# Kernel tuning notes

Hardware: AMD Instinct MI355X
Metric: run time of the kernel (lower is better)

The kernel has to match this reference:

```python
import jax, jax.numpy as jnp
import numpy as np

HEAD, DIM_IN, HDIM = 8, 256, 64
B, N = 4, 2048


def setup_inputs() -> dict:
    key = jax.random.key(0)
    k1, k2, k3, k4 = jax.random.split(key, 4)
    # xavier_uniform gain=1.414 bounds
    def xavier(k, shape, fan_in, fan_out):
        bound = 1.414 * np.sqrt(6.0 / (fan_in + fan_out))
        return jax.random.uniform(k, shape, jnp.float32, -bound, bound)
    h = jax.random.normal(k1, (B, N, DIM_IN), jnp.float32)
    w = xavier(k2, (HEAD, DIM_IN, HDIM), DIM_IN, HDIM)
    a_src = xavier(k3, (HEAD, HDIM, 1), HDIM, 1)
    a_dst = xavier(k4, (HEAD, HDIM, 1), HDIM, 1)
    b = jnp.zeros((HDIM,), jnp.float32)
    return {"h": h, "w": w, "a_src": a_src, "a_dst": a_dst, "b": b}


def reference(h, w, a_src, a_dst, b):
    # h: [B,N,Din], w: [H,Din,O] -> h_: [B,H,N,O]
    h_ = jnp.einsum("bnd,hdo->bhno", h, w)
    # additive attention logits per node: [B,H,N]
    src = jnp.einsum("bhno,ho->bhn", h_, a_src[..., 0])
    dst = jnp.einsum("bhno,ho->bhn", h_, a_dst[..., 0])
    # attn[b,h,i,j] = leaky_relu(src[i] + dst[j]); softmax over j
    logits = jax.nn.leaky_relu(src[..., :, None] + dst[..., None, :], negative_slope=0.2)
    attn = jax.nn.softmax(logits, axis=-1)  # [B,H,N,N]
    h_out = jnp.einsum("bhij,bhjo->bhio", attn, h_)
    return h_out + b
```

## Files before the change

kernel.cpp:

```cpp
#include <hip/hip_runtime.h>
#include <cstdint>
#include <cstddef>


#define HEADS 8
#define DIN   256
#define HDIM  64
#define NN    2048

typedef __attribute__((ext_vector_type(8))) _Float16 f16x8;
typedef __attribute__((ext_vector_type(2))) _Float16 f16x2;
typedef __attribute__((ext_vector_type(2))) __fp16   fp16x2;
typedef __attribute__((ext_vector_type(4))) float f32x4;

union H8 { f16x8 v; f16x2 p[4]; unsigned u[4]; };
union F2U { f16x2 h; fp16x2 q; unsigned u; };

__device__ __forceinline__ f16x2 pkrtz(float a, float b) {
  F2U t; t.q = __builtin_amdgcn_cvt_pkrtz(a, b);
  return t.h;
}
__device__ __forceinline__ unsigned pkrtz_u(float a, float b) {
  F2U t; t.q = __builtin_amdgcn_cvt_pkrtz(a, b);
  return t.u;
}

__global__ __launch_bounds__(256) void gat_prep(const float* __restrict__ w,
                                                const float* __restrict__ h,
                                                _Float16* __restrict__ wt,
                                                _Float16* __restrict__ hc) {
  const int bid = blockIdx.x;
  if (bid < 512) {
    const int idx = bid * 256 + threadIdx.x;
    const int o  = idx & 63;
    const int k  = (idx >> 6) & 255;
    const int hd = idx >> 14;
    wt[(hd * HDIM + o) * DIN + k] = (_Float16)w[idx];
  } else {
    const int idx = (bid - 512) * 256 + threadIdx.x;
    const float* p = h + (size_t)idx * 8;
    float4 x0 = ((const float4*)p)[0];
    float4 x1 = ((const float4*)p)[1];
    H8 o;
    o.p[0] = pkrtz(x0.x, x0.y); o.p[1] = pkrtz(x0.z, x0.w);
    o.p[2] = pkrtz(x1.x, x1.y); o.p[3] = pkrtz(x1.z, x1.w);
    *(f16x8*)(hc + (size_t)idx * 8) = o.v;
  }
}

__global__ __launch_bounds__(256) void gat_proj(const _Float16* __restrict__ hc,
                                                const _Float16* __restrict__ wt,
                                                const float* __restrict__ a_src,
                                                const float* __restrict__ a_dst,
                                                _Float16* __restrict__ h_t,
                                                float* __restrict__ src_s,
                                                float* __restrict__ dst_s) {
  const int head = blockIdx.x;
  const int rt   = blockIdx.y;
  const int tid  = threadIdx.x;
  const int w    = tid >> 6;
  const int lane = tid & 63;
  const int l15  = lane & 15, lg = lane >> 4;

  const int rowg = rt * 128 + w * 32;
  const _Float16* hb = hc + (size_t)rowg * DIN;
  const _Float16* wb = wt + head * (HDIM * DIN);

  f32x4 acc[2][4] = {};
#pragma unroll
  for (int kk = 0; kk < 8; ++kk) {
    const int k0 = kk * 32 + lg * 8;
    f16x8 af[2];
#pragma unroll
    for (int m = 0; m < 2; ++m)
      af[m] = *(const f16x8*)(hb + (size_t)(m * 16 + l15) * DIN + k0);
    f16x8 bfr[4];
#pragma unroll
    for (int n = 0; n < 4; ++n)
      bfr[n] = *(const f16x8*)(wb + (size_t)(n * 16 + l15) * DIN + k0);
#pragma unroll
    for (int m = 0; m < 2; ++m)
#pragma unroll
      for (int n = 0; n < 4; ++n)
        acc[m][n] = __builtin_amdgcn_mfma_f32_16x16x32_f16(af[m], bfr[n], acc[m][n], 0, 0, 0);
  }

  const int b   = (rt * 128) >> 11;
  const int nl0 = ((rt * 128) & 2047) + w * 32;
  const int bh  = b * HEADS + head;
  _Float16* hb_t = h_t + (size_t)bh * (256 * 512);
#pragma unroll
  for (int m = 0; m < 2; ++m)
#pragma unroll
    for (int n = 0; n < 4; ++n) {
      uint2 pk;
      pk.x = pkrtz_u(acc[m][n][0], acc[m][n][1]);
      pk.y = pkrtz_u(acc[m][n][2], acc[m][n][3]);
      const int j0 = nl0 + m * 16 + lg * 4;
      const int o  = n * 16 + l15;
      *(uint2*)(hb_t + (size_t)(j0 >> 3) * 512 + o * 8 + (j0 & 7)) = pk;
    }

  const float LOG2E = 1.4426950408889634f;
  float as4[4], ad4[4];
#pragma unroll
  for (int n = 0; n < 4; ++n) {
    as4[n] = a_src[head * HDIM + n * 16 + l15];
    ad4[n] = a_dst[head * HDIM + n * 16 + l15];
  }
#pragma unroll
  for (int m = 0; m < 2; ++m)
#pragma unroll
    for (int reg = 0; reg < 4; ++reg) {
      float ps = 0.f, pd = 0.f;
#pragma unroll
      for (int n = 0; n < 4; ++n) {
        float c = acc[m][n][reg];
        ps = fmaf(c, as4[n], ps);
        pd = fmaf(c, ad4[n], pd);
      }
#pragma unroll
      for (int off = 1; off <= 8; off <<= 1) {
        ps += __shfl_xor(ps, off);
        pd += __shfl_xor(pd, off);
      }
      if (l15 == 0) {
        const int nl = nl0 + m * 16 + lg * 4 + reg;
        src_s[(size_t)bh * NN + nl] = ps * LOG2E;
        dst_s[(size_t)bh * NN + nl] = pd * LOG2E;
      }
    }
}

__global__ __launch_bounds__(256) void gat_flash(const float* __restrict__ src_s,
                                                 const float* __restrict__ dst_s,
                                                 const _Float16* __restrict__ h_t,
                                                 const float* __restrict__ bias,
                                                 float* __restrict__ out) {
  const int it  = blockIdx.x;
  const int bh  = blockIdx.y;
  const int tid = threadIdx.x;
  const int w   = tid >> 6;
  const int lane = tid & 63;
  const int l15 = lane & 15, lg = lane >> 4;

  __shared__ _Float16 Ef[NN];
  __shared__ _Float16 Ff[NN];
  __shared__ float red[4];

  const float* dstp = dst_s + (size_t)bh * NN;
  const _Float16* vpan = h_t + (size_t)bh * (256 * 512);
  const _Float16* fb = vpan + lg * 512 + l15 * 8;

  float d[8];
  {
    float4 q0 = *(const float4*)(dstp + tid * 8);
    float4 q1 = *(const float4*)(dstp + tid * 8 + 4);
    d[0]=q0.x; d[1]=q0.y; d[2]=q0.z; d[3]=q0.w;
    d[4]=q1.x; d[5]=q1.y; d[6]=q1.z; d[7]=q1.w;
  }
  float dm = fmaxf(fmaxf(fmaxf(d[0],d[1]),fmaxf(d[2],d[3])),
                   fmaxf(fmaxf(d[4],d[5]),fmaxf(d[6],d[7])));
#pragma unroll
  for (int off = 32; off >= 1; off >>= 1) dm = fmaxf(dm, __shfl_xor(dm, off));
  if (lane == 0) red[w] = dm;
  __syncthreads();
  dm = fmaxf(fmaxf(red[0], red[1]), fmaxf(red[2], red[3]));

  {
    H8 e8, f8;
#pragma unroll
    for (int k = 0; k < 4; ++k) {
      float a0 = d[2*k]   - dm;
      float a1 = d[2*k+1] - dm;
      e8.p[k] = pkrtz(__builtin_amdgcn_exp2f(a0), __builtin_amdgcn_exp2f(a1));
      f8.p[k] = pkrtz(__builtin_amdgcn_exp2f(0.2f * a0),
                      __builtin_amdgcn_exp2f(0.2f * a1));
    }
    *(f16x8*)(&Ef[tid * 8]) = e8.v;
    *(f16x8*)(&Ff[tid * 8]) = f8.v;
  }
  __syncthreads();

  const float* srcp = src_s + (size_t)bh * NN + it * 128 + w * 32;
  f16x2 u2[2], v2[2];
#pragma unroll
  for (int m = 0; m < 2; ++m) {
    float sv   = srcp[m * 16 + l15];
    float smax = sv + dm;
    float mi   = fmaxf(smax, 0.2f * smax);
    float u    = __builtin_amdgcn_exp2f(smax - mi);
    float v    = __builtin_amdgcn_exp2f(fmaf(0.2f, smax, -mi));
    u2[m] = pkrtz(u, u);
    v2[m] = pkrtz(v, v);
  }

  f32x4 acc[2][4] = {};
  f32x4 accs[2]   = {};
  H8 onesU; onesU.u[0] = onesU.u[1] = onesU.u[2] = onesU.u[3] = 0x3C003C00u;
  const f16x8 ones = onesU.v;

  f16x8 V00, V01, V02, V03, V10, V11, V12, V13;
  f16x8 V20, V21, V22, V23, V30, V31, V32, V33;

#define LOADV(s, jc) do {                                              \
    const _Float16* fp_ = fb + (size_t)(jc) * 2048;                    \
    V##s##0 = *(const f16x8*)(fp_);                                    \
    V##s##1 = *(const f16x8*)(fp_ + 128);                              \
    V##s##2 = *(const f16x8*)(fp_ + 256);                              \
    V##s##3 = *(const f16x8*)(fp_ + 384);                              \
  } while (0)

#define STEP(s, jc) do {                                               \
    H8 eu_, fu_;                                                       \
    eu_.v = *(const f16x8*)(&Ef[(jc) * 32 + lg * 8]);                  \
    fu_.v = *(const f16x8*)(&Ff[(jc) * 32 + lg * 8]);                  \
    _Pragma("unroll") for (int m = 0; m < 2; ++m) {                    \
      H8 af_;                                                          \
      af_.p[0] = __builtin_elementwise_max(u2[m] * eu_.p[0], v2[m] * fu_.p[0]); \
      af_.p[1] = __builtin_elementwise_max(u2[m] * eu_.p[1], v2[m] * fu_.p[1]); \
      af_.p[2] = __builtin_elementwise_max(u2[m] * eu_.p[2], v2[m] * fu_.p[2]); \
      af_.p[3] = __builtin_elementwise_max(u2[m] * eu_.p[3], v2[m] * fu_.p[3]); \
      acc[m][0] = __builtin_amdgcn_mfma_f32_16x16x32_f16(af_.v, V##s##0, acc[m][0], 0, 0, 0); \
      acc[m][1] = __builtin_amdgcn_mfma_f32_16x16x32_f16(af_.v, V##s##1, acc[m][1], 0, 0, 0); \
      acc[m][2] = __builtin_amdgcn_mfma_f32_16x16x32_f16(af_.v, V##s##2, acc[m][2], 0, 0, 0); \
      acc[m][3] = __builtin_amdgcn_mfma_f32_16x16x32_f16(af_.v, V##s##3, acc[m][3], 0, 0, 0); \
      accs[m]   = __builtin_amdgcn_mfma_f32_16x16x32_f16(af_.v, ones, accs[m], 0, 0, 0);      \
    }                                                                  \
  } while (0)

  LOADV(0, 0);
  LOADV(1, 1);
  LOADV(2, 2);
#pragma unroll 1
  for (int t = 0; t < 60; t += 4) {
    LOADV(3, t + 3); STEP(0, t);
    LOADV(0, t + 4); STEP(1, t + 1);
    LOADV(1, t + 5); STEP(2, t + 2);
    LOADV(2, t + 6); STEP(3, t + 3);
  }
  LOADV(3, 63);
  STEP(0, 60); STEP(1, 61); STEP(2, 62); STEP(3, 63);

#undef LOADV
#undef STEP

  float bb[4];
#pragma unroll
  for (int n = 0; n < 4; ++n) bb[n] = bias[n * 16 + l15];

  float* ob = out + ((size_t)bh * NN + it * 128 + w * 32) * HDIM;
#pragma unroll
  for (int m = 0; m < 2; ++m)
#pragma unroll
    for (int reg = 0; reg < 4; ++reg) {
      const float linv = 1.0f / accs[m][reg];
      const int r = m * 16 + lg * 4 + reg;
#pragma unroll
      for (int n = 0; n < 4; ++n)
        ob[(size_t)r * HDIM + n * 16 + l15] = fmaf(acc[m][n][reg], linv, bb[n]);
    }
}

extern "C" void kernel_launch(void* const* d_in, const int* in_sizes, int n_in,
                              void* d_out, int out_size, void* d_ws, size_t ws_size,
                              hipStream_t stream) {
  const float* h     = (const float*)d_in[0];
  const float* w     = (const float*)d_in[1];
  const float* a_src = (const float*)d_in[2];
  const float* a_dst = (const float*)d_in[3];
  const float* bias  = (const float*)d_in[4];
  float* out = (float*)d_out;

  char* ws = (char*)d_ws;
  _Float16* wt  = (_Float16*)ws;
  _Float16* h_t = (_Float16*)(ws + 262144);
  float* src_s = (float*)(ws + 262144 + 8388608);
  float* dst_s = (float*)(ws + 262144 + 8388608 + 262144);

  _Float16* hcv = (_Float16*)d_out;

  hipLaunchKernelGGL(gat_prep,  dim3(1536),   dim3(256), 0, stream, w, h, wt, hcv);
  hipLaunchKernelGGL(gat_proj,  dim3(8, 64),  dim3(256), 0, stream,
                     hcv, wt, a_src, a_dst, h_t, src_s, dst_s);
  hipLaunchKernelGGL(gat_flash, dim3(16, 32), dim3(256), 0, stream,
                     src_s, dst_s, h_t, bias, out);
}
```

Before: 49.58 us.

## Deepen V-fragment prefetch to eight stages and prioritize MFMA issue

Raises the register-level software pipeline for V fragments from four to eight slots, so global loads are issued seven chunks ahead instead of three. The STEP body now computes both attention-fragment operands before issuing all ten MFMAs in one burst, and wraps that burst in s_setprio to raise wave priority. The aim is to hide more global load latency and keep the matrix unit busy. The cost is 64 extra VGPRs for V buffers, which could lower occupancy or cause spills.

```diff
diff --git a/kernel.cpp b/kernel.cpp
--- a/kernel.cpp
+++ b/kernel.cpp
@@ -202,6 +202,8 @@
 
   f16x8 V00, V01, V02, V03, V10, V11, V12, V13;
   f16x8 V20, V21, V22, V23, V30, V31, V32, V33;
+  f16x8 V40, V41, V42, V43, V50, V51, V52, V53;
+  f16x8 V60, V61, V62, V63, V70, V71, V72, V73;
 
 #define LOADV(s, jc) do {                                              \
     const _Float16* fp_ = fb + (size_t)(jc) * 2048;                    \
@@ -215,32 +217,45 @@
     H8 eu_, fu_;                                                       \
     eu_.v = *(const f16x8*)(&Ef[(jc) * 32 + lg * 8]);                  \
     fu_.v = *(const f16x8*)(&Ff[(jc) * 32 + lg * 8]);                  \
-    _Pragma("unroll") for (int m = 0; m < 2; ++m) {                    \
-      H8 af_;                                                          \
-      af_.p[0] = __builtin_elementwise_max(u2[m] * eu_.p[0], v2[m] * fu_.p[0]); \
-      af_.p[1] = __builtin_elementwise_max(u2[m] * eu_.p[1], v2[m] * fu_.p[1]); \
-      af_.p[2] = __builtin_elementwise_max(u2[m] * eu_.p[2], v2[m] * fu_.p[2]); \
-      af_.p[3] = __builtin_elementwise_max(u2[m] * eu_.p[3], v2[m] * fu_.p[3]); \
-      acc[m][0] = __builtin_amdgcn_mfma_f32_16x16x32_f16(af_.v, V##s##0, acc[m][0], 0, 0, 0); \
-      acc[m][1] = __builtin_amdgcn_mfma_f32_16x16x32_f16(af_.v, V##s##1, acc[m][1], 0, 0, 0); \
-      acc[m][2] = __builtin_amdgcn_mfma_f32_16x16x32_f16(af_.v, V##s##2, acc[m][2], 0, 0, 0); \
-      acc[m][3] = __builtin_amdgcn_mfma_f32_16x16x32_f16(af_.v, V##s##3, acc[m][3], 0, 0, 0); \
-      accs[m]   = __builtin_amdgcn_mfma_f32_16x16x32_f16(af_.v, ones, accs[m], 0, 0, 0);      \
-    }                                                                  \
+    H8 af0_, af1_;                                                     \
+    af0_.p[0] = __builtin_elementwise_max(u2[0] * eu_.p[0], v2[0] * fu_.p[0]); \
+    af0_.p[1] = __builtin_elementwise_max(u2[0] * eu_.p[1], v2[0] * fu_.p[1]); \
+    af0_.p[2] = __builtin_elementwise_max(u2[0] * eu_.p[2], v2[0] * fu_.p[2]); \
+    af0_.p[3] = __builtin_elementwise_max(u2[0] * eu_.p[3], v2[0] * fu_.p[3]); \
+    af1_.p[0] = __builtin_elementwise_max(u2[1] * eu_.p[0], v2[1] * fu_.p[0]); \
+    af1_.p[1] = __builtin_elementwise_max(u2[1] * eu_.p[1], v2[1] * fu_.p[1]); \
+    af1_.p[2] = __builtin_elementwise_max(u2[1] * eu_.p[2], v2[1] * fu_.p[2]); \
+    af1_.p[3] = __builtin_elementwise_max(u2[1] * eu_.p[3], v2[1] * fu_.p[3]); \
+    __builtin_amdgcn_s_setprio(1);                                     \
+    acc[0][0] = __builtin_amdgcn_mfma_f32_16x16x32_f16(af0_.v, V##s##0, acc[0][0], 0, 0, 0); \
+    acc[0][1] = __builtin_amdgcn_mfma_f32_16x16x32_f16(af0_.v, V##s##1, acc[0][1], 0, 0, 0); \
+    acc[0][2] = __builtin_amdgcn_mfma_f32_16x16x32_f16(af0_.v, V##s##2, acc[0][2], 0, 0, 0); \
+    acc[0][3] = __builtin_amdgcn_mfma_f32_16x16x32_f16(af0_.v, V##s##3, acc[0][3], 0, 0, 0); \
+    accs[0]   = __builtin_amdgcn_mfma_f32_16x16x32_f16(af0_.v, ones, accs[0], 0, 0, 0);      \
+    acc[1][0] = __builtin_amdgcn_mfma_f32_16x16x32_f16(af1_.v, V##s##0, acc[1][0], 0, 0, 0); \
+    acc[1][1] = __builtin_amdgcn_mfma_f32_16x16x32_f16(af1_.v, V##s##1, acc[1][1], 0, 0, 0); \
+    acc[1][2] = __builtin_amdgcn_mfma_f32_16x16x32_f16(af1_.v, V##s##2, acc[1][2], 0, 0, 0); \
+    acc[1][3] = __builtin_amdgcn_mfma_f32_16x16x32_f16(af1_.v, V##s##3, acc[1][3], 0, 0, 0); \
+    accs[1]   = __builtin_amdgcn_mfma_f32_16x16x32_f16(af1_.v, ones, accs[1], 0, 0, 0);      \
+    __builtin_amdgcn_s_setprio(0);                                     \
   } while (0)
 
-  LOADV(0, 0);
-  LOADV(1, 1);
-  LOADV(2, 2);
+  LOADV(0, 0); LOADV(1, 1); LOADV(2, 2); LOADV(3, 3);
+  LOADV(4, 4); LOADV(5, 5); LOADV(6, 6);
 #pragma unroll 1
-  for (int t = 0; t < 60; t += 4) {
-    LOADV(3, t + 3); STEP(0, t);
-    LOADV(0, t + 4); STEP(1, t + 1);
-    LOADV(1, t + 5); STEP(2, t + 2);
-    LOADV(2, t + 6); STEP(3, t + 3);
-  }
-  LOADV(3, 63);
-  STEP(0, 60); STEP(1, 61); STEP(2, 62); STEP(3, 63);
+  for (int t = 0; t < 56; t += 8) {
+    LOADV(7, t + 7);  STEP(0, t);
+    LOADV(0, t + 8);  STEP(1, t + 1);
+    LOADV(1, t + 9);  STEP(2, t + 2);
+    LOADV(2, t + 10); STEP(3, t + 3);
+    LOADV(3, t + 11); STEP(4, t + 4);
+    LOADV(4, t + 12); STEP(5, t + 5);
+    LOADV(5, t + 13); STEP(6, t + 6);
+    LOADV(6, t + 14); STEP(7, t + 7);
+  }
+  LOADV(7, 63);
+  STEP(0, 56); STEP(1, 57); STEP(2, 58); STEP(3, 59);
+  STEP(4, 60); STEP(5, 61); STEP(6, 62); STEP(7, 63);
 
 #undef LOADV
 #undef STEP
```

After: 50.28 us. No clear change (+1.4%).

## Split key range across warp pairs in flash kernel and reduce partials via LDS

Applied to the files above, without the earlier changes.

Each block now covers 64 query rows instead of 128, and the four warps split into two row groups times two halves of the key range. Partial outputs and row sums from the second half are passed through shared memory and added by the first half before normalisation. The grid doubles to 1024 blocks, the V prefetch drops from four stages to three, and launch bounds ask for four blocks per CU. Together these aim to raise occupancy and parallelism at the cost of extra LDS, a barrier, and half the warps sitting idle during the epilogue.

```diff
diff --git a/kernel.cpp b/kernel.cpp
--- a/kernel.cpp
+++ b/kernel.cpp
@@ -132,25 +132,44 @@
     }
 }
 
-__global__ __launch_bounds__(256) void gat_flash(const float* __restrict__ src_s,
-                                                 const float* __restrict__ dst_s,
-                                                 const _Float16* __restrict__ h_t,
-                                                 const float* __restrict__ bias,
-                                                 float* __restrict__ out) {
+__global__ __launch_bounds__(256, 4) void gat_flash(const float* __restrict__ src_s,
+                                                    const float* __restrict__ dst_s,
+                                                    const _Float16* __restrict__ h_t,
+                                                    const float* __restrict__ bias,
+                                                    float* __restrict__ out) {
   const int it  = blockIdx.x;
   const int bh  = blockIdx.y;
   const int tid = threadIdx.x;
   const int w   = tid >> 6;
   const int lane = tid & 63;
   const int l15 = lane & 15, lg = lane >> 4;
+  const int rg  = w >> 1;
+  const int jh  = w & 1;
 
   __shared__ _Float16 Ef[NN];
   __shared__ _Float16 Ff[NN];
+  __shared__ f32x4 Oc[2][2][4][64];
+  __shared__ f32x4 Sc[2][2][64];
   __shared__ float red[4];
 
   const float* dstp = dst_s + (size_t)bh * NN;
   const _Float16* vpan = h_t + (size_t)bh * (256 * 512);
   const _Float16* fb = vpan + lg * 512 + l15 * 8;
+  const int jb = jh * 32;
+
+  f16x8 V00, V01, V02, V03, V10, V11, V12, V13, V20, V21, V22, V23;
+
+#define LOADV(s, jc) do {                                              \
+    const _Float16* fp_ = fb + (size_t)(jc) * 2048;                    \
+    V##s##0 = *(const f16x8*)(fp_);                                    \
+    V##s##1 = *(const f16x8*)(fp_ + 128);                              \
+    V##s##2 = *(const f16x8*)(fp_ + 256);                              \
+    V##s##3 = *(const f16x8*)(fp_ + 384);                              \
+  } while (0)
+
+  LOADV(0, jb + 0);
+  LOADV(1, jb + 1);
+  LOADV(2, jb + 2);
 
   float d[8];
   {
@@ -182,7 +201,7 @@
   }
   __syncthreads();
 
-  const float* srcp = src_s + (size_t)bh * NN + it * 128 + w * 32;
+  const float* srcp = src_s + (size_t)bh * NN + it * 64 + rg * 32;
   f16x2 u2[2], v2[2];
 #pragma unroll
   for (int m = 0; m < 2; ++m) {
@@ -199,17 +218,6 @@
   f32x4 accs[2]   = {};
   H8 onesU; onesU.u[0] = onesU.u[1] = onesU.u[2] = onesU.u[3] = 0x3C003C00u;
   const f16x8 ones = onesU.v;
-
-  f16x8 V00, V01, V02, V03, V10, V11, V12, V13;
-  f16x8 V20, V21, V22, V23, V30, V31, V32, V33;
-
-#define LOADV(s, jc) do {                                              \
-    const _Float16* fp_ = fb + (size_t)(jc) * 2048;                    \
-    V##s##0 = *(const f16x8*)(fp_);                                    \
-    V##s##1 = *(const f16x8*)(fp_ + 128);                              \
-    V##s##2 = *(const f16x8*)(fp_ + 256);                              \
-    V##s##3 = *(const f16x8*)(fp_ + 384);                              \
-  } while (0)
 
 #define STEP(s, jc) do {                                               \
     H8 eu_, fu_;                                                       \
@@ -229,37 +237,51 @@
     }                                                                  \
   } while (0)
 
-  LOADV(0, 0);
-  LOADV(1, 1);
-  LOADV(2, 2);
 #pragma unroll 1
-  for (int t = 0; t < 60; t += 4) {
-    LOADV(3, t + 3); STEP(0, t);
-    LOADV(0, t + 4); STEP(1, t + 1);
-    LOADV(1, t + 5); STEP(2, t + 2);
-    LOADV(2, t + 6); STEP(3, t + 3);
-  }
-  LOADV(3, 63);
-  STEP(0, 60); STEP(1, 61); STEP(2, 62); STEP(3, 63);
+  for (int t = 0; t < 27; t += 3) {
+    STEP(0, jb + t);     LOADV(0, jb + t + 3);
+    STEP(1, jb + t + 1); LOADV(1, jb + t + 4);
+    STEP(2, jb + t + 2); LOADV(2, jb + t + 5);
+  }
+  STEP(0, jb + 27); LOADV(0, jb + 30);
+  STEP(1, jb + 28); LOADV(1, jb + 31);
+  STEP(2, jb + 29);
+  STEP(0, jb + 30);
+  STEP(1, jb + 31);
 
 #undef LOADV
 #undef STEP
 
-  float bb[4];
-#pragma unroll
-  for (int n = 0; n < 4; ++n) bb[n] = bias[n * 16 + l15];
-
-  float* ob = out + ((size_t)bh * NN + it * 128 + w * 32) * HDIM;
-#pragma unroll
-  for (int m = 0; m < 2; ++m)
-#pragma unroll
-    for (int reg = 0; reg < 4; ++reg) {
-      const float linv = 1.0f / accs[m][reg];
-      const int r = m * 16 + lg * 4 + reg;
-#pragma unroll
-      for (int n = 0; n < 4; ++n)
-        ob[(size_t)r * HDIM + n * 16 + l15] = fmaf(acc[m][n][reg], linv, bb[n]);
-    }
+  if (jh == 1) {
+#pragma unroll
+    for (int m = 0; m < 2; ++m) {
+      Sc[rg][m][lane] = accs[m];
+#pragma unroll
+      for (int n = 0; n < 4; ++n) Oc[rg][m][n][lane] = acc[m][n];
+    }
+  }
+  __syncthreads();
+  if (jh == 0) {
+    float bb[4];
+#pragma unroll
+    for (int n = 0; n < 4; ++n) bb[n] = bias[n * 16 + l15];
+
+    float* ob = out + ((size_t)bh * NN + it * 64 + rg * 32) * HDIM;
+#pragma unroll
+    for (int m = 0; m < 2; ++m) {
+      f32x4 st = accs[m] + Sc[rg][m][lane];
+#pragma unroll
+      for (int reg = 0; reg < 4; ++reg) {
+        const float linv = 1.0f / st[reg];
+        const int r = m * 16 + lg * 4 + reg;
+#pragma unroll
+        for (int n = 0; n < 4; ++n) {
+          float o = acc[m][n][reg] + Oc[rg][m][n][lane][reg];
+          ob[(size_t)r * HDIM + n * 16 + l15] = fmaf(o, linv, bb[n]);
+        }
+      }
+    }
+  }
 }
 
 extern "C" void kernel_launch(void* const* d_in, const int* in_sizes, int n_in,
@@ -283,6 +305,6 @@
   hipLaunchKernelGGL(gat_prep,  dim3(1536),   dim3(256), 0, stream, w, h, wt, hcv);
   hipLaunchKernelGGL(gat_proj,  dim3(8, 64),  dim3(256), 0, stream,
                      hcv, wt, a_src, a_dst, h_t, src_s, dst_s);
-  hipLaunchKernelGGL(gat_flash, dim3(16, 32), dim3(256), 0, stream,
+  hipLaunchKernelGGL(gat_flash, dim3(32, 32), dim3(256), 0, stream,
                      src_s, dst_s, h_t, bias, out);
 }
```

Result: slower. 59.17 us (+19.3%).
